# Kernel tuning notes

Hardware: AMD Instinct MI355X
Metric: run time of the kernel (lower is better)

## Reference

```python
import jax, jax.numpy as jnp
import numpy as np

NS, L, H = 8, 2048, 1024
M, E, K = 4096, 8, 2
EPS = 1e-9

def setup_inputs() -> dict:
    key = jax.random.key(0)
    ks = jax.random.split(key, 5)
    s = 0.02
    return {
        "x": jax.random.normal(ks[0], (NS, L, H), jnp.float32),
        "Wr": jax.random.normal(ks[1], (H, E), jnp.float32) * s,
        "br": jnp.zeros((E,), jnp.float32),
        "W1": jax.random.normal(ks[2], (E, H, M), jnp.float32) * s,
        "b1": jnp.zeros((E, M), jnp.float32),
        "W2": jax.random.normal(ks[3], (E, M, H), jnp.float32) * s,
        "b2": jnp.zeros((E, H), jnp.float32),
    }

def reference(x, Wr, br, W1, b1, W2, b2):
    ns, seq, h = x.shape
    flat = x.reshape(-1, h)                      # (N, H); grouping only reshapes, math is per-token
    logits = flat @ Wr + br                      # (N, E)
    probs = jax.nn.softmax(logits, axis=-1)
    vals, idx = jax.lax.top_k(probs, K)          # (N, K)
    w = vals / (jnp.sum(vals, axis=-1, keepdims=True) + EPS)
    out_acc = jnp.zeros_like(flat)
    weight_acc = jnp.zeros((flat.shape[0],), flat.dtype)
    for e in range(E):                           # fixed small expert loop
        we = jnp.sum(w * (idx == e), axis=-1)    # (N,) combine weight for expert e
        hmid = jax.nn.gelu(flat @ W1[e] + b1[e], approximate=False)
        y = hmid @ W2[e] + b2[e]
        out_acc = out_acc + we[:, None] * y
        weight_acc = weight_acc + we
    out = out_acc / (weight_acc[:, None] + EPS)
    return out.reshape(ns, seq, h)
```

## Files before the change

kernel.cpp:

```cpp
#include <hip/hip_runtime.h>
#include <hip/hip_bf16.h>
#include <math.h>

#define NTOK 16384
#define HDIM 1024
#define MDIM 4096
#define NEXP 8
#define EPSV 1e-9f
#define RTOK 32

typedef unsigned short u16;
typedef __attribute__((ext_vector_type(4))) float f32x4;
typedef __attribute__((ext_vector_type(8))) __bf16 bf16x8;
typedef __attribute__((ext_vector_type(8))) unsigned short u16x8;
typedef __attribute__((ext_vector_type(4))) unsigned short u16x4;

#define ASYNC_COPY16(gptr, lptr) \
    __builtin_amdgcn_global_load_lds( \
        (const __attribute__((address_space(1))) void*)(gptr), \
        (__attribute__((address_space(3))) void*)(lptr), 16, 0, 0)

static __device__ __forceinline__ u16 f2bf(float f) {
    unsigned int u = __builtin_bit_cast(unsigned int, f);
    u += 0x7fff + ((u >> 16) & 1);
    return (u16)(u >> 16);
}

static __device__ __forceinline__ float gelu_f(float v) {
    float z2 = -1.5957691216f * v * (1.f + 0.044715f * v * v);
    return v / (1.f + __expf(z2));
}

__global__ __launch_bounds__(256) void router_kernel(
    const float* __restrict__ x, const float* __restrict__ Wr,
    const float* __restrict__ br,
    int* __restrict__ counts, int* __restrict__ ltok, float* __restrict__ lcf,
    u16* __restrict__ xb)
{
    __shared__ int   lcount[NEXP];
    __shared__ int   lbase[NEXP];
    __shared__ int   ltokL[NEXP][RTOK];
    __shared__ float lcfL[NEXP][RTOK];

    int t = threadIdx.x;
    if (t < NEXP) lcount[t] = 0;
    __syncthreads();

    int wave = t >> 6, lane = t & 63;

    for (int it = 0; it < RTOK / 4; ++it) {
        int tok = blockIdx.x * RTOK + it * 4 + wave;
        const float* xr = x + (size_t)tok * HDIM + lane * 16;

        f32x4 xv[4];
        #pragma unroll
        for (int q = 0; q < 4; q++) xv[q] = *reinterpret_cast<const f32x4*>(xr + q * 4);

        u16x8 ob0, ob1;
        #pragma unroll
        for (int j = 0; j < 4; j++) {
            ob0[j]     = f2bf(xv[0][j]);
            ob0[4 + j] = f2bf(xv[1][j]);
            ob1[j]     = f2bf(xv[2][j]);
            ob1[4 + j] = f2bf(xv[3][j]);
        }
        u16* xo = xb + (size_t)tok * HDIM + lane * 16;
        *reinterpret_cast<u16x8*>(xo)     = ob0;
        *reinterpret_cast<u16x8*>(xo + 8) = ob1;

        f32x4 acc0 = {0.f, 0.f, 0.f, 0.f};
        f32x4 acc1 = {0.f, 0.f, 0.f, 0.f};
        #pragma unroll
        for (int q = 0; q < 4; q++) {
            #pragma unroll
            for (int j = 0; j < 4; j++) {
                int h = lane * 16 + q * 4 + j;
                const float* wrow = Wr + (size_t)h * NEXP;
                f32x4 w0 = *reinterpret_cast<const f32x4*>(wrow);
                f32x4 w1 = *reinterpret_cast<const f32x4*>(wrow + 4);
                acc0 += xv[q][j] * w0;
                acc1 += xv[q][j] * w1;
            }
        }
        float a[NEXP];
        #pragma unroll
        for (int e = 0; e < 4; e++) { a[e] = acc0[e]; a[4 + e] = acc1[e]; }
        #pragma unroll
        for (int e = 0; e < NEXP; e++) {
            #pragma unroll
            for (int s = 1; s < 64; s <<= 1) a[e] += __shfl_xor(a[e], s, 64);
        }
        if (lane == 0) {
            float l[NEXP], m = -1e30f;
            #pragma unroll
            for (int e = 0; e < NEXP; e++) { l[e] = a[e] + br[e]; m = fmaxf(m, l[e]); }
            float p[NEXP], s = 0.f;
            #pragma unroll
            for (int e = 0; e < NEXP; e++) { p[e] = expf(l[e] - m); s += p[e]; }
            int i0 = 0; float v0 = p[0];
            #pragma unroll
            for (int e = 1; e < NEXP; e++) if (p[e] > v0) { v0 = p[e]; i0 = e; }
            int i1 = -1; float v1 = -1.f;
            #pragma unroll
            for (int e = 0; e < NEXP; e++) if (e != i0 && p[e] > v1) { v1 = p[e]; i1 = e; }
            v0 /= s; v1 /= s;
            float sw = v0 + v1;
            float w0 = v0 / (sw + EPSV), w1 = v1 / (sw + EPSV);
            float wa = w0 + w1;
            float c0 = w0 / (wa + EPSV), c1 = w1 / (wa + EPSV);
            int q0 = atomicAdd(&lcount[i0], 1);
            ltokL[i0][q0] = tok; lcfL[i0][q0] = c0;
            int q1 = atomicAdd(&lcount[i1], 1);
            ltokL[i1][q1] = tok; lcfL[i1][q1] = c1;
        }
    }
    __syncthreads();
    if (t < NEXP) lbase[t] = atomicAdd(&counts[t], lcount[t]);
    __syncthreads();
    #pragma unroll
    for (int e = 0; e < NEXP; e++) {
        int n = lcount[e], b = lbase[e];
        for (int j = t; j < n; j += 256) {
            ltok[e * NTOK + b + j] = ltokL[e][j];
            lcf[e * NTOK + b + j]  = lcfL[e][j];
        }
    }
}

__global__ void bases_kernel(const int* __restrict__ counts, int* __restrict__ bases)
{
    if (threadIdx.x == 0) {
        int acc = 0;
        #pragma unroll
        for (int e = 0; e < NEXP; e++) { bases[e] = acc; acc += counts[e]; }
    }
}

__global__ __launch_bounds__(256) void transpose_cvt_kernel(
    const float* __restrict__ W1, const float* __restrict__ W2,
    u16* __restrict__ w1t, u16* __restrict__ w2t)
{
    __shared__ float tile[32][33];
    int z = blockIdx.z;
    int R, C;
    const float* ine;
    u16* oute;
    if (z < NEXP) {
        R = HDIM; C = MDIM;
        ine  = W1 + (size_t)z * R * C;
        oute = w1t + (size_t)z * R * C;
    } else {
        R = MDIM; C = HDIM;
        ine  = W2 + (size_t)(z - NEXP) * R * C;
        oute = w2t + (size_t)(z - NEXP) * R * C;
    }
    int tiles_x = C >> 5;
    int ti = blockIdx.x;
    int c0 = (ti & (tiles_x - 1)) * 32;
    int r0 = (ti / tiles_x) * 32;

    int t = threadIdx.x;
    int r = t >> 3, cq = t & 7;
    f32x4 v = *reinterpret_cast<const f32x4*>(ine + (size_t)(r0 + r) * C + c0 + cq * 4);
    #pragma unroll
    for (int j = 0; j < 4; j++) tile[r][cq * 4 + j] = v[j];
    __syncthreads();
    int c = t >> 3, rq = t & 7;
    u16x4 o;
    #pragma unroll
    for (int j = 0; j < 4; j++) o[j] = f2bf(tile[rq * 4 + j][c]);
    *reinterpret_cast<u16x4*>(oute + (size_t)(c0 + c) * R + r0 + rq * 4) = o;
}

template<int EPI, int NSPLIT, int GX, int GY>
__global__ __launch_bounds__(512) void gemm_kernel(
    const u16* __restrict__ A,
    const u16* __restrict__ BT_all,
    const float* __restrict__ bias_all,
    const int* __restrict__ counts,
    const int* __restrict__ bases,
    const int* __restrict__ ltok,
    const float* __restrict__ lcf,
    u16* __restrict__ hmid,
    float* __restrict__ out,
    int K, int P, int Astride, int eStart)
{
    int gz = gridDim.z;
    int nwg = GX * GY * gz;
    int orig = blockIdx.x + GX * (blockIdx.y + GY * blockIdx.z);
    int qq = nwg >> 3, rr = nwg & 7;
    int xcd = orig & 7, sub = orig >> 3;
    int wgid = (xcd < rr ? xcd * (qq + 1) : rr * (qq + 1) + (xcd - rr) * qq) + sub;
    int bx = wgid & (GX - 1);
    int rem = wgid / GX;
    int by = rem & (GY - 1);
    int bz = rem / GY;

    int e   = eStart + (NSPLIT > 1 ? (bz / NSPLIT) : bz);
    int spl = (NSPLIT > 1) ? (bz % NSPLIT) : 0;
    int nrows = counts[e];
    int row0 = by * 256;
    if (row0 >= nrows) return;
    int p0 = bx * 128;
    int slotbase = bases[e];
    const u16*   BT   = BT_all + (size_t)e * P * K;
    const float* bias = bias_all + (size_t)e * P;
    const int*   lte  = ltok + (size_t)e * NTOK;
    const float* lcfe = lcf  + (size_t)e * NTOK;

    int kseg = K / NSPLIT;
    int ks0 = spl * kseg, ks1 = ks0 + kseg;

    __shared__ u16 As[256][64];
    __shared__ u16 Bs[128][64];

    int t = threadIdx.x;
    int wv = t >> 6, lane = t & 63;
    int lrow8 = lane >> 3;
    int lcol8 = lane & 7;
    int schunk = lcol8 ^ lrow8;

    const u16* aptr[4];
    const u16* bptr[2];
    #pragma unroll
    for (int i = 0; i < 4; i++) {
        int pos  = row0 + wv * 32 + i * 8 + lrow8;
        int posc = min(pos, nrows - 1);
        int arow = (EPI == 0) ? lte[posc] : (slotbase + posc);
        aptr[i] = A + (size_t)arow * Astride + schunk * 8;
    }
    #pragma unroll
    for (int j = 0; j < 2; j++) {
        int prow = p0 + wv * 16 + j * 8 + lrow8;
        bptr[j] = BT + (size_t)prow * K + schunk * 8;
    }

    int wr = (wv >> 1) * 64, wc = (wv & 1) * 64;
    int lr = lane & 15, lg = lane >> 4;
    int lr7 = lr & 7;

    f32x4 acc[4][4];
    #pragma unroll
    for (int m = 0; m < 4; m++)
        #pragma unroll
        for (int nn = 0; nn < 4; nn++) acc[m][nn] = (f32x4){0.f, 0.f, 0.f, 0.f};

    for (int k0 = ks0; k0 < ks1; k0 += 64) {
        #pragma unroll
        for (int i = 0; i < 4; i++)
            ASYNC_COPY16(aptr[i] + k0, &As[wv * 32 + i * 8][0]);
        #pragma unroll
        for (int j = 0; j < 2; j++)
            ASYNC_COPY16(bptr[j] + k0, &Bs[wv * 16 + j * 8][0]);
        __syncthreads();
        #pragma unroll
        for (int kk = 0; kk < 64; kk += 32) {
            int q = kk >> 3;
            bf16x8 af[4], bf[4];
            #pragma unroll
            for (int m = 0; m < 4; m++)
                af[m] = *reinterpret_cast<const bf16x8*>(
                    &As[wr + m * 16 + lr][((q + lg) ^ lr7) * 8]);
            #pragma unroll
            for (int nn = 0; nn < 4; nn++)
                bf[nn] = *reinterpret_cast<const bf16x8*>(
                    &Bs[wc + nn * 16 + lr][((q + lg) ^ lr7) * 8]);
            #pragma unroll
            for (int m = 0; m < 4; m++)
                #pragma unroll
                for (int nn = 0; nn < 4; nn++)
                    acc[m][nn] = __builtin_amdgcn_mfma_f32_16x16x32_bf16(
                        af[m], bf[nn], acc[m][nn], 0, 0, 0);
        }
        __syncthreads();
    }

    if (EPI == 0) {
        #pragma unroll
        for (int m = 0; m < 4; m++) {
            #pragma unroll
            for (int r2 = 0; r2 < 4; r2++) {
                int pos = row0 + wr + m * 16 + lg * 4 + r2;
                if (pos < nrows) {
                    size_t ho = (size_t)(slotbase + pos) * MDIM;
                    #pragma unroll
                    for (int nn = 0; nn < 4; nn++) {
                        int col = p0 + wc + nn * 16 + lr;
                        float v = acc[m][nn][r2] + bias[col];
                        hmid[ho + col] = f2bf(gelu_f(v));
                    }
                }
            }
        }
    } else {
        #pragma unroll
        for (int m = 0; m < 4; m++) {
            #pragma unroll
            for (int r2 = 0; r2 < 4; r2++) {
                int pos = row0 + wr + m * 16 + lg * 4 + r2;
                if (pos < nrows) {
                    int tokr = lte[pos];
                    float cf = lcfe[pos];
                    float* orow = out + (size_t)tokr * HDIM;
                    #pragma unroll
                    for (int nn = 0; nn < 4; nn++) {
                        int col = p0 + wc + nn * 16 + lr;
                        float bb = (spl == 0) ? bias[col] : 0.f;
                        float v = (acc[m][nn][r2] + bb) * cf;
                        atomicAdd(orow + col, v);
                    }
                }
            }
        }
    }
}

extern "C" void kernel_launch(void* const* d_in, const int* in_sizes, int n_in,
                              void* d_out, int out_size, void* d_ws, size_t ws_size,
                              hipStream_t stream)
{
    const float* x  = (const float*)d_in[0];
    const float* Wr = (const float*)d_in[1];
    const float* br = (const float*)d_in[2];
    const float* W1 = (const float*)d_in[3];
    const float* b1 = (const float*)d_in[4];
    const float* W2 = (const float*)d_in[5];
    const float* b2 = (const float*)d_in[6];
    float* out = (float*)d_out;

    char* ws = (char*)d_ws;
    size_t off = 0;
    auto alloc = [&](size_t bytes) {
        void* p = ws + off;
        off = (off + bytes + 255) & ~(size_t)255;
        return p;
    };
    int*   counts = (int*)  alloc(NEXP * 4);
    int*   bases  = (int*)  alloc(NEXP * 4);
    int*   ltok   = (int*)  alloc((size_t)NEXP * NTOK * 4);
    float* lcf    = (float*)alloc((size_t)NEXP * NTOK * 4);
    u16*   xb     = (u16*)  alloc((size_t)NTOK * HDIM * 2);
    u16*   w1t    = (u16*)  alloc((size_t)NEXP * MDIM * HDIM * 2);
    u16*   w2t    = (u16*)  alloc((size_t)NEXP * HDIM * MDIM * 2);
    size_t fixed_end = off;
    bool grouped = (ws_size >= fixed_end + (size_t)2 * NTOK * MDIM * 2);
    u16* hmid = (u16*)alloc((grouped ? (size_t)2 * NTOK : (size_t)NTOK) * MDIM * 2);

    hipMemsetAsync(counts, 0, NEXP * 4, stream);
    hipMemsetAsync(d_out, 0, (size_t)out_size * sizeof(float), stream);

    transpose_cvt_kernel<<<dim3((HDIM * MDIM) / 1024, 1, 2 * NEXP), 256, 0, stream>>>(
        W1, W2, w1t, w2t);
    router_kernel<<<NTOK / RTOK, 256, 0, stream>>>(x, Wr, br, counts, ltok, lcf, xb);

    if (grouped) {
        bases_kernel<<<1, 64, 0, stream>>>(counts, bases);
        gemm_kernel<0, 1, MDIM / 128, NTOK / 256>
            <<<dim3(MDIM / 128, NTOK / 256, NEXP), 512, 0, stream>>>(
            xb, w1t, b1, counts, bases, ltok, lcf, hmid, nullptr,
            HDIM, MDIM, HDIM, 0);
        gemm_kernel<1, 2, HDIM / 128, NTOK / 256>
            <<<dim3(HDIM / 128, NTOK / 256, NEXP * 2), 512, 0, stream>>>(
            hmid, w2t, b2, counts, bases, ltok, lcf, nullptr, out,
            MDIM, HDIM, MDIM, 0);
    } else {
        hipMemsetAsync(bases, 0, NEXP * 4, stream);
        for (int e = 0; e < NEXP; e++) {
            gemm_kernel<0, 1, MDIM / 128, NTOK / 256>
                <<<dim3(MDIM / 128, NTOK / 256, 1), 512, 0, stream>>>(
                xb, w1t, b1, counts, bases, ltok, lcf, hmid, nullptr,
                HDIM, MDIM, HDIM, e);
            gemm_kernel<1, 1, HDIM / 128, NTOK / 256>
                <<<dim3(HDIM / 128, NTOK / 256, 1), 512, 0, stream>>>(
                hmid, w2t, b2, counts, bases, ltok, lcf, nullptr, out,
                MDIM, HDIM, MDIM, e);
        }
    }
}
```

Baseline: 1.019 ms.

## Halve GEMM K-tile to 32 and drop split-K on second expert GEMM

The K step per iteration shrinks from 64 to 32, halving LDS tiles and rewriting the async-copy mapping and XOR swizzle for 4 chunks per row. Split-K on the down-projection GEMM is removed, so each block covers the full K range and the bias is always added. This lowers LDS use, which may allow more blocks per CU, and halves the atomic adds to the output. The cost is twice as many barriers per unit of K and half the blocks for the second GEMM.

```diff
diff --git a/kernel.cpp b/kernel.cpp
--- a/kernel.cpp
+++ b/kernel.cpp
@@ -172,7 +172,7 @@
     *reinterpret_cast<u16x4*>(oute + (size_t)(c0 + c) * R + r0 + rq * 4) = o;
 }
 
-template<int EPI, int NSPLIT, int GX, int GY>
+template<int EPI, int GX, int GY>
 __global__ __launch_bounds__(512) void gemm_kernel(
     const u16* __restrict__ A,
     const u16* __restrict__ BT_all,
@@ -196,8 +196,7 @@
     int by = rem & (GY - 1);
     int bz = rem / GY;
 
-    int e   = eStart + (NSPLIT > 1 ? (bz / NSPLIT) : bz);
-    int spl = (NSPLIT > 1) ? (bz % NSPLIT) : 0;
+    int e = eStart + bz;
     int nrows = counts[e];
     int row0 = by * 256;
     if (row0 >= nrows) return;
@@ -208,36 +207,28 @@
     const int*   lte  = ltok + (size_t)e * NTOK;
     const float* lcfe = lcf  + (size_t)e * NTOK;
 
-    int kseg = K / NSPLIT;
-    int ks0 = spl * kseg, ks1 = ks0 + kseg;
-
-    __shared__ u16 As[256][64];
-    __shared__ u16 Bs[128][64];
+    __shared__ u16 As[256][32];
+    __shared__ u16 Bs[128][32];
 
     int t = threadIdx.x;
     int wv = t >> 6, lane = t & 63;
-    int lrow8 = lane >> 3;
-    int lcol8 = lane & 7;
-    int schunk = lcol8 ^ lrow8;
-
-    const u16* aptr[4];
-    const u16* bptr[2];
-    #pragma unroll
-    for (int i = 0; i < 4; i++) {
-        int pos  = row0 + wv * 32 + i * 8 + lrow8;
+
+    int rl = t >> 2, ch = t & 3;
+    int sc = ch ^ ((rl >> 1) & 3);
+    const u16* aptr[2];
+    const u16* bptr;
+    #pragma unroll
+    for (int i = 0; i < 2; i++) {
+        int pos  = row0 + i * 128 + rl;
         int posc = min(pos, nrows - 1);
         int arow = (EPI == 0) ? lte[posc] : (slotbase + posc);
-        aptr[i] = A + (size_t)arow * Astride + schunk * 8;
-    }
-    #pragma unroll
-    for (int j = 0; j < 2; j++) {
-        int prow = p0 + wv * 16 + j * 8 + lrow8;
-        bptr[j] = BT + (size_t)prow * K + schunk * 8;
-    }
+        aptr[i] = A + (size_t)arow * Astride + sc * 8;
+    }
+    bptr = BT + (size_t)(p0 + rl) * K + sc * 8;
 
     int wr = (wv >> 1) * 64, wc = (wv & 1) * 64;
     int lr = lane & 15, lg = lane >> 4;
-    int lr7 = lr & 7;
+    int rsw = (lg ^ ((lr >> 1) & 3)) * 8;
 
     f32x4 acc[4][4];
     #pragma unroll
@@ -245,33 +236,26 @@
         #pragma unroll
         for (int nn = 0; nn < 4; nn++) acc[m][nn] = (f32x4){0.f, 0.f, 0.f, 0.f};
 
-    for (int k0 = ks0; k0 < ks1; k0 += 64) {
-        #pragma unroll
-        for (int i = 0; i < 4; i++)
-            ASYNC_COPY16(aptr[i] + k0, &As[wv * 32 + i * 8][0]);
-        #pragma unroll
-        for (int j = 0; j < 2; j++)
-            ASYNC_COPY16(bptr[j] + k0, &Bs[wv * 16 + j * 8][0]);
+    for (int k0 = 0; k0 < K; k0 += 32) {
+        #pragma unroll
+        for (int i = 0; i < 2; i++)
+            ASYNC_COPY16(aptr[i] + k0, &As[i * 128 + wv * 16][0]);
+        ASYNC_COPY16(bptr + k0, &Bs[wv * 16][0]);
         __syncthreads();
-        #pragma unroll
-        for (int kk = 0; kk < 64; kk += 32) {
-            int q = kk >> 3;
-            bf16x8 af[4], bf[4];
-            #pragma unroll
-            for (int m = 0; m < 4; m++)
-                af[m] = *reinterpret_cast<const bf16x8*>(
-                    &As[wr + m * 16 + lr][((q + lg) ^ lr7) * 8]);
+
+        bf16x8 af[4], bf[4];
+        #pragma unroll
+        for (int m = 0; m < 4; m++)
+            af[m] = *reinterpret_cast<const bf16x8*>(&As[wr + m * 16 + lr][rsw]);
+        #pragma unroll
+        for (int nn = 0; nn < 4; nn++)
+            bf[nn] = *reinterpret_cast<const bf16x8*>(&Bs[wc + nn * 16 + lr][rsw]);
+        #pragma unroll
+        for (int m = 0; m < 4; m++)
             #pragma unroll
             for (int nn = 0; nn < 4; nn++)
-                bf[nn] = *reinterpret_cast<const bf16x8*>(
-                    &Bs[wc + nn * 16 + lr][((q + lg) ^ lr7) * 8]);
-            #pragma unroll
-            for (int m = 0; m < 4; m++)
-                #pragma unroll
-                for (int nn = 0; nn < 4; nn++)
-                    acc[m][nn] = __builtin_amdgcn_mfma_f32_16x16x32_bf16(
-                        af[m], bf[nn], acc[m][nn], 0, 0, 0);
-        }
+                acc[m][nn] = __builtin_amdgcn_mfma_f32_16x16x32_bf16(
+                    af[m], bf[nn], acc[m][nn], 0, 0, 0);
         __syncthreads();
     }
 
@@ -305,8 +289,7 @@
                     #pragma unroll
                     for (int nn = 0; nn < 4; nn++) {
                         int col = p0 + wc + nn * 16 + lr;
-                        float bb = (spl == 0) ? bias[col] : 0.f;
-                        float v = (acc[m][nn][r2] + bb) * cf;
+                        float v = (acc[m][nn][r2] + bias[col]) * cf;
                         atomicAdd(orow + col, v);
                     }
                 }
@@ -355,22 +338,22 @@
 
     if (grouped) {
         bases_kernel<<<1, 64, 0, stream>>>(counts, bases);
-        gemm_kernel<0, 1, MDIM / 128, NTOK / 256>
+        gemm_kernel<0, MDIM / 128, NTOK / 256>
             <<<dim3(MDIM / 128, NTOK / 256, NEXP), 512, 0, stream>>>(
             xb, w1t, b1, counts, bases, ltok, lcf, hmid, nullptr,
             HDIM, MDIM, HDIM, 0);
-        gemm_kernel<1, 2, HDIM / 128, NTOK / 256>
-            <<<dim3(HDIM / 128, NTOK / 256, NEXP * 2), 512, 0, stream>>>(
+        gemm_kernel<1, HDIM / 128, NTOK / 256>
+            <<<dim3(HDIM / 128, NTOK / 256, NEXP), 512, 0, stream>>>(
             hmid, w2t, b2, counts, bases, ltok, lcf, nullptr, out,
             MDIM, HDIM, MDIM, 0);
     } else {
         hipMemsetAsync(bases, 0, NEXP * 4, stream);
         for (int e = 0; e < NEXP; e++) {
-            gemm_kernel<0, 1, MDIM / 128, NTOK / 256>
+            gemm_kernel<0, MDIM / 128, NTOK / 256>
                 <<<dim3(MDIM / 128, NTOK / 256, 1), 512, 0, stream>>>(
                 xb, w1t, b1, counts, bases, ltok, lcf, hmid, nullptr,
                 HDIM, MDIM, HDIM, e);
-            gemm_kernel<1, 1, HDIM / 128, NTOK / 256>
+            gemm_kernel<1, HDIM / 128, NTOK / 256>
                 <<<dim3(HDIM / 128, NTOK / 256, 1), 512, 0, stream>>>(
                 hmid, w2t, b2, counts, bases, ltok, lcf, nullptr, out,
                 MDIM, HDIM, MDIM, e);
```

After: 1.041 ms. 1.02x slower.
